# Optimization experiments

Hardware: AMD Instinct MI355X
Metric: run time of the kernel (lower is better)

## Reference

```python
import jax, jax.numpy as jnp
import numpy as np

T, B, I, H = 512, 64, 1024, 1024


def setup_inputs() -> dict:
    key = jax.random.key(0)
    ks = jax.random.split(key, 16)
    d = {
        "inputs": jax.random.normal(ks[0], (T, B, I), dtype=jnp.float32),
        "hx": jnp.zeros((B, H), dtype=jnp.float32),
        "cx": jnp.zeros((B, H), dtype=jnp.float32),
        # weights [H, I] / [H, H] as in nn.Parameter(torch.randn(...)); scaled down for stability
        "w_ii": jax.random.normal(ks[1], (H, I), jnp.float32) * 0.02,
        "w_fi": jax.random.normal(ks[2], (H, I), jnp.float32) * 0.02,
        "w_ai": jax.random.normal(ks[3], (H, I), jnp.float32) * 0.02,
        "w_oi": jax.random.normal(ks[4], (H, I), jnp.float32) * 0.02,
        "w_ih": jax.random.normal(ks[5], (H, H), jnp.float32) * 0.02,
        "w_fh": jax.random.normal(ks[6], (H, H), jnp.float32) * 0.02,
        "w_ah": jax.random.normal(ks[7], (H, H), jnp.float32) * 0.02,
        "w_oh": jax.random.normal(ks[8], (H, H), jnp.float32) * 0.02,
        "b_i": jax.random.uniform(ks[9], (H,), jnp.float32),
        "b_f": jax.random.uniform(ks[10], (H,), jnp.float32),
        "b_a": jax.random.uniform(ks[11], (H,), jnp.float32),
        "b_o": jax.random.normal(ks[12], (H,), jnp.float32),
    }
    return d


def reference(inputs, hx, cx, w_ii, w_fi, w_ai, w_oi, w_ih, w_fh, w_ah, w_oh,
              b_i, b_f, b_a, b_o):
    # FP quant type -> weight proxies and quant activations are identity;
    # layer_norm='identity'; rec_quant/out_quant are IdentityQuant.
    # Stack the 4 gate matrices so each step does one [B,I]x[I,4H] and one
    # [B,H]x[H,4H] GEMM (same math as the 8 separate torch.mm calls).
    Wi = jnp.concatenate([w_ii, w_fi, w_ai, w_oi], axis=0).T  # [I, 4H]
    Wh = jnp.concatenate([w_ih, w_fh, w_ah, w_oh], axis=0).T  # [H, 4H]
    b = jnp.concatenate([b_i, b_f, b_a, b_o], axis=0)          # [4H]
    Hh = hx.shape[-1]

    def step(carry, x_t):
        h, c = carry
        gates = x_t @ Wi + h @ Wh + b                 # [B, 4H]
        i_g, f_g, a_g, o_g = jnp.split(gates, 4, axis=-1)
        i_g = jax.nn.sigmoid(i_g)
        f_g = jax.nn.sigmoid(f_g)
        a_g = jnp.tanh(a_g)
        o_g = jax.nn.sigmoid(o_g)
        cy = f_g * c + i_g * a_g
        hy = o_g * jnp.tanh(cy)
        return (hy, cy), hy

    (hy, cy), outputs = jax.lax.scan(step, (hx, cx), inputs)
    return outputs, hy, cy
```

## Files before the change

kernel.cpp:

```cpp
#include <hip/hip_runtime.h>
#include <cstdint>

typedef _Float16 half8 __attribute__((ext_vector_type(8)));
typedef _Float16 half4v __attribute__((ext_vector_type(4)));
typedef float floatx4 __attribute__((ext_vector_type(4)));
typedef unsigned long long u64;

__device__ __forceinline__ float sig_(float x) { return 1.f / (1.f + __expf(-x)); }
__device__ __forceinline__ float tanh_(float x) {
  x = fminf(15.f, fmaxf(-15.f, x));
  float e = __expf(2.f * x);
  return (e - 1.f) / (e + 1.f);
}

__global__ void cvt_x_kernel(const float* __restrict__ x, _Float16* __restrict__ xh, int n) {
  int i = (blockIdx.x * 256 + threadIdx.x) * 4;
  if (i < n) {
    const float4 v = *(const float4*)(x + i);
    half4v o = {(_Float16)v.x, (_Float16)v.y, (_Float16)v.z, (_Float16)v.w};
    *(half4v*)(xh + i) = o;
  }
}

__global__ void build_w_kernel(const float* w0, const float* w1, const float* w2, const float* w3,
                               const float* w4, const float* w5, const float* w6, const float* w7,
                               const float* b0, const float* b1, const float* b2, const float* b3,
                               _Float16* __restrict__ Wip, _Float16* __restrict__ Whp,
                               float* __restrict__ biasp) {
  int n = blockIdx.x;
  if (n < 8192) {
    const float* srcs[8] = {w0, w1, w2, w3, w4, w5, w6, w7};
    int which = n >> 12;
    int row = n & 4095;
    int u = row >> 2, g = row & 3;
    const float* s = srcs[which * 4 + g] + (size_t)u * 1024;
    _Float16* dst = (which ? Whp : Wip) + (size_t)row * 1024;
    int t = threadIdx.x * 4;
    float4 v = *(const float4*)(s + t);
    half4v o = {(_Float16)v.x, (_Float16)v.y, (_Float16)v.z, (_Float16)v.w};
    *(half4v*)(dst + t) = o;
  } else {
    const float* bs[4] = {b0, b1, b2, b3};
    for (int idx = threadIdx.x; idx < 4096; idx += 256)
      biasp[idx] = bs[idx & 3][idx >> 2];
  }
}

__global__ void init_h_kernel(const float* __restrict__ hx, unsigned int* __restrict__ hbuf) {
  int i = blockIdx.x * 256 + threadIdx.x;
  if (i < 32768) {
    unsigned short lo = __builtin_bit_cast(unsigned short, (_Float16)hx[2 * i]);
    unsigned short hi = __builtin_bit_cast(unsigned short, (_Float16)hx[2 * i + 1]);
    hbuf[i] = (unsigned int)lo | ((unsigned int)hi << 16);
  }
}

__global__ void zero_flags_kernel(unsigned int* __restrict__ flags) {
  int i = blockIdx.x * 256 + threadIdx.x;
  if (i < 8192) flags[i] = 0u;
}

__global__ __launch_bounds__(256) void gemm_g_kernel(const _Float16* __restrict__ Xh,
                                                     const _Float16* __restrict__ Wp,
                                                     const float* __restrict__ biasp,
                                                     _Float16* __restrict__ G3) {
  __shared__ _Float16 Al[4][128][8];
  __shared__ _Float16 Bl[4][128][8];
  const int tid = threadIdx.x;
  const int w = tid >> 6, l = tid & 63;
  const int wm = (w >> 1) * 64, wn = (w & 1) * 64;
  const int ml = l & 15, kg = l >> 4;
  const int bm = blockIdx.x, bn = blockIdx.y;
  const int r0 = tid & 127, kc0 = tid >> 7;
  const int kc1 = kc0 + 2;
  const size_t arow0 = (size_t)(bm * 128 + r0) * 1024;
  const size_t brow0 = (size_t)(bn * 128 + r0) * 1024;
  floatx4 acc[4][4] = {};
  for (int kt = 0; kt < 1024; kt += 32) {
    __syncthreads();
    __builtin_amdgcn_global_load_lds(
        (const __attribute__((address_space(1))) unsigned int*)(Xh + arow0 + kt + kc0 * 8),
        (__attribute__((address_space(3))) unsigned int*)&Al[kc0][r0][0], 16, 0, 0);
    __builtin_amdgcn_global_load_lds(
        (const __attribute__((address_space(1))) unsigned int*)(Xh + arow0 + kt + kc1 * 8),
        (__attribute__((address_space(3))) unsigned int*)&Al[kc1][r0][0], 16, 0, 0);
    __builtin_amdgcn_global_load_lds(
        (const __attribute__((address_space(1))) unsigned int*)(Wp + brow0 + kt + kc0 * 8),
        (__attribute__((address_space(3))) unsigned int*)&Bl[kc0][r0][0], 16, 0, 0);
    __builtin_amdgcn_global_load_lds(
        (const __attribute__((address_space(1))) unsigned int*)(Wp + brow0 + kt + kc1 * 8),
        (__attribute__((address_space(3))) unsigned int*)&Bl[kc1][r0][0], 16, 0, 0);
    __syncthreads();
    half8 af[4], bf[4];
#pragma unroll
    for (int i = 0; i < 4; ++i) af[i] = *(const half8*)&Al[kg][wm + i * 16 + ml][0];
#pragma unroll
    for (int j = 0; j < 4; ++j) bf[j] = *(const half8*)&Bl[kg][wn + j * 16 + ml][0];
#pragma unroll
    for (int i = 0; i < 4; ++i)
#pragma unroll
      for (int j = 0; j < 4; ++j)
        acc[i][j] = __builtin_amdgcn_mfma_f32_16x16x32_f16(af[i], bf[j], acc[i][j], 0, 0, 0);
  }
  const int t = (bm * 128 + wm) >> 6;
#pragma unroll
  for (int j = 0; j < 4; ++j) {
    const int col = bn * 128 + wn + j * 16 + ml;
    const float bj = biasp[col];
    const int p = col >> 4;
#pragma unroll
    for (int i = 0; i < 4; ++i) {
      half4v pk = {(_Float16)(acc[i][j][0] + bj), (_Float16)(acc[i][j][1] + bj),
                   (_Float16)(acc[i][j][2] + bj), (_Float16)(acc[i][j][3] + bj)};
      *(half4v*)&G3[((size_t)p * 512 + t) * 1024 + i * 256 + kg * 64 + ml * 4] = pk;
    }
  }
}

__global__ __launch_bounds__(256, 1) void lstm_rec_kernel(
    const _Float16* __restrict__ G3, const _Float16* __restrict__ Whp,
    unsigned int* __restrict__ hbuf, const float* __restrict__ cx,
    float* __restrict__ out, unsigned int* __restrict__ flags) {
  const int p = blockIdx.x, tid = threadIdx.x;
  const int w = tid >> 6, l = tid & 63;
  const int ml = l & 15, kg = l >> 4;
  __shared__ _Float16 hl_[32768];
  char* hl = (char*)(hl_ + w * 8192);

  half8 wfr[32];
#pragma unroll
  for (int s = 0; s < 32; ++s)
    wfr[s] = *(const half8*)&Whp[(size_t)(16 * p + ml) * 1024 + s * 32 + kg * 8];

  const int bl = l >> 2, u = l & 3;
  const int bglob = 16 * w + bl, U = 4 * p + u;
  float c = cx[bglob * 1024 + U];
  __syncthreads();

  for (int t = 0; t < 512; ++t) {
    const u64* hq = (const u64*)(hbuf + (size_t)(t & 1) * 32768);
    u64* hnq = (u64*)(hbuf + (size_t)((t & 1) ^ 1) * 32768);

    u64 c1[32], c2[32];
#pragma unroll
    for (int i = 0; i < 32; ++i) {
      const int row = i >> 1, j = ((i & 1) << 6) + l;
      c1[i] = __hip_atomic_load(&hq[(size_t)(16 * w + row) * 256 + j], __ATOMIC_RELAXED,
                                __HIP_MEMORY_SCOPE_AGENT);
    }
    const u64 ginb =
        *(const u64*)&G3[((size_t)p * 512 + t) * 1024 + w * 256 + kg * 64 + ml * 4];
#pragma unroll
    for (int i = 0; i < 32; ++i) {
      const int row = i >> 1, j = ((i & 1) << 6) + l;
      c2[i] = __hip_atomic_load(&hq[(size_t)(16 * w + row) * 256 + 128 + j], __ATOMIC_RELAXED,
                                __HIP_MEMORY_SCOPE_AGENT);
    }

#pragma unroll
    for (int i = 0; i < 32; ++i) {
      const int row = i >> 1, j = ((i & 1) << 6) + l;
      const int un = (j >> 1) ^ (row & 7);
      *(u64*)(hl + row * 1024 + un * 16 + (j & 1) * 8) = c1[i];
    }
    __builtin_amdgcn_wave_barrier();
    floatx4 acc[4] = {};
#pragma unroll
    for (int s = 0; s < 16; ++s) {
      const int un = (s * 4 + kg) ^ (ml & 7);
      half8 a = *(const half8*)(hl + ml * 1024 + un * 16);
      acc[s & 3] = __builtin_amdgcn_mfma_f32_16x16x32_f16(a, wfr[s], acc[s & 3], 0, 0, 0);
    }
    __builtin_amdgcn_wave_barrier();
#pragma unroll
    for (int i = 0; i < 32; ++i) {
      const int row = i >> 1, j = ((i & 1) << 6) + l;
      const int un = (j >> 1) ^ (row & 7);
      *(u64*)(hl + row * 1024 + un * 16 + (j & 1) * 8) = c2[i];
    }
    __builtin_amdgcn_wave_barrier();
#pragma unroll
    for (int s = 0; s < 16; ++s) {
      const int un = (s * 4 + kg) ^ (ml & 7);
      half8 a = *(const half8*)(hl + ml * 1024 + un * 16);
      acc[s & 3] = __builtin_amdgcn_mfma_f32_16x16x32_f16(a, wfr[16 + s], acc[s & 3], 0, 0, 0);
    }
    floatx4 a4 = (acc[0] + acc[1]) + (acc[2] + acc[3]);

    union { u64 q; half4v h4; } gu; gu.q = ginb;
    float* glw = (float*)hl;
    __builtin_amdgcn_wave_barrier();
#pragma unroll
    for (int r = 0; r < 4; ++r)
      glw[(kg * 4 + r) * 20 + ml] = a4[r] + (float)gu.h4[r];
    __builtin_amdgcn_wave_barrier();
    const float4 g4 = *(const float4*)&glw[bl * 20 + u * 4];

    const float ig = sig_(g4.x), fg = sig_(g4.y);
    const float ag = tanh_(g4.z), og = sig_(g4.w);
    c = fg * c + ig * ag;
    const float h = og * tanh_(c);

    unsigned int mine = (unsigned int)__builtin_bit_cast(unsigned short, (_Float16)h);
    unsigned int pair = mine | (((unsigned int)__shfl_xor((int)mine, 1)) << 16);
    u64 quad = (u64)pair | ((u64)(unsigned int)__shfl_xor((int)pair, 2) << 32);
    if (u == 0)
      __hip_atomic_store(&hnq[(size_t)bglob * 256 + p], quad, __ATOMIC_RELAXED,
                         __HIP_MEMORY_SCOPE_AGENT);

    if (t == 511) {
      out[(size_t)t * 65536 + bglob * 1024 + U] = h;
      out[(size_t)33554432 + bglob * 1024 + U] = h;
      out[(size_t)33619968 + bglob * 1024 + U] = c;
      break;
    }

    __builtin_amdgcn_s_waitcnt(0x0F70);
    __syncthreads();
    if (tid == 0)
      __hip_atomic_store(&flags[p * 32], (unsigned)(t + 1), __ATOMIC_RELAXED,
                         __HIP_MEMORY_SCOPE_AGENT);
    out[(size_t)t * 65536 + bglob * 1024 + U] = h;
    const unsigned tgt = (unsigned)(t + 1);
    int done;
    do {
      unsigned v = __hip_atomic_load(&flags[tid * 32], __ATOMIC_RELAXED,
                                     __HIP_MEMORY_SCOPE_AGENT);
      done = __syncthreads_and((int)(v >= tgt));
      if (!done) __builtin_amdgcn_s_sleep(2);
    } while (!done);
    asm volatile("" ::: "memory");
  }
}

extern "C" void kernel_launch(void* const* d_in, const int* in_sizes, int n_in,
                              void* d_out, int out_size, void* d_ws, size_t ws_size,
                              hipStream_t stream) {
  const float* x    = (const float*)d_in[0];
  const float* hx   = (const float*)d_in[1];
  const float* cxp  = (const float*)d_in[2];
  const float* w_ii = (const float*)d_in[3];
  const float* w_fi = (const float*)d_in[4];
  const float* w_ai = (const float*)d_in[5];
  const float* w_oi = (const float*)d_in[6];
  const float* w_ih = (const float*)d_in[7];
  const float* w_fh = (const float*)d_in[8];
  const float* w_ah = (const float*)d_in[9];
  const float* w_oh = (const float*)d_in[10];
  const float* b_i  = (const float*)d_in[11];
  const float* b_f  = (const float*)d_in[12];
  const float* b_a  = (const float*)d_in[13];
  const float* b_o  = (const float*)d_in[14];
  float* out = (float*)d_out;

  char* ws = (char*)d_ws;
  _Float16* Xh        = (_Float16*)(ws);
  unsigned int* flags = (unsigned int*)(ws);
  _Float16* Wip       = (_Float16*)(ws + 67108864);
  _Float16* Whp       = (_Float16*)(ws + 75497472);
  float* biasp        = (float*)(ws + 83886080);
  unsigned int* hbuf  = (unsigned int*)(ws + 83902464);
  _Float16* G3        = (_Float16*)(ws + 84164864);
  if (ws_size < (size_t)84164864 + 268435456) return;

  cvt_x_kernel<<<32768, 256, 0, stream>>>(x, Xh, 33554432);
  build_w_kernel<<<8193, 256, 0, stream>>>(w_ii, w_fi, w_ai, w_oi, w_ih, w_fh, w_ah, w_oh,
                                           b_i, b_f, b_a, b_o, Wip, Whp, biasp);
  init_h_kernel<<<128, 256, 0, stream>>>(hx, hbuf);
  gemm_g_kernel<<<dim3(256, 32), 256, 0, stream>>>(Xh, Wip, biasp, G3);
  zero_flags_kernel<<<32, 256, 0, stream>>>(flags);
  lstm_rec_kernel<<<256, 256, 0, stream>>>(G3, Whp, hbuf, cxp, out, flags);
}
```

Measured before the change: 3.805 ms.

## Load hidden state directly into LDS with pre-swizzled layout and faster flag polling

```diff
diff --git a/kernel.cpp b/kernel.cpp
--- a/kernel.cpp
+++ b/kernel.cpp
@@ -46,12 +46,16 @@
   }
 }
 
-__global__ void init_h_kernel(const float* __restrict__ hx, unsigned int* __restrict__ hbuf) {
+__global__ void init_h_kernel(const float* __restrict__ hx, char* __restrict__ hb0) {
   int i = blockIdx.x * 256 + threadIdx.x;
   if (i < 32768) {
-    unsigned short lo = __builtin_bit_cast(unsigned short, (_Float16)hx[2 * i]);
-    unsigned short hi = __builtin_bit_cast(unsigned short, (_Float16)hx[2 * i + 1]);
-    hbuf[i] = (unsigned int)lo | ((unsigned int)hi << 16);
+    int r = i >> 9, j = i & 511;
+    int c = j >> 8, xoff = (j & 255) * 4;
+    int o = (xoff + r * 16) & 1023;
+    unsigned short lo = __builtin_bit_cast(unsigned short, (_Float16)hx[r * 1024 + 2 * j]);
+    unsigned short hi = __builtin_bit_cast(unsigned short, (_Float16)hx[r * 1024 + 2 * j + 1]);
+    *(unsigned int*)(hb0 + (size_t)r * 2048 + c * 1024 + o) =
+        (unsigned int)lo | ((unsigned int)hi << 16);
   }
 }
 
@@ -119,13 +123,13 @@
 
 __global__ __launch_bounds__(256, 1) void lstm_rec_kernel(
     const _Float16* __restrict__ G3, const _Float16* __restrict__ Whp,
-    unsigned int* __restrict__ hbuf, const float* __restrict__ cx,
+    char* __restrict__ hbuf, const float* __restrict__ cx,
     float* __restrict__ out, unsigned int* __restrict__ flags) {
   const int p = blockIdx.x, tid = threadIdx.x;
   const int w = tid >> 6, l = tid & 63;
   const int ml = l & 15, kg = l >> 4;
-  __shared__ _Float16 hl_[32768];
-  char* hl = (char*)(hl_ + w * 8192);
+  __shared__ char hl_[65536] __attribute__((aligned(16)));
+  char* slice = hl_ + w * 16384;
 
   half8 wfr[32];
 #pragma unroll
@@ -135,60 +139,43 @@
   const int bl = l >> 2, u = l & 3;
   const int bglob = 16 * w + bl, U = 4 * p + u;
   float c = cx[bglob * 1024 + U];
+  const int rot = kg * 16 + ml * 16 + w * 256;
   __syncthreads();
 
+  u64 ginb = *(const u64*)&G3[((size_t)p * 512 + 0) * 1024 + w * 256 + kg * 64 + ml * 4];
+
   for (int t = 0; t < 512; ++t) {
-    const u64* hq = (const u64*)(hbuf + (size_t)(t & 1) * 32768);
-    u64* hnq = (u64*)(hbuf + (size_t)((t & 1) ^ 1) * 32768);
-
-    u64 c1[32], c2[32];
-#pragma unroll
-    for (int i = 0; i < 32; ++i) {
-      const int row = i >> 1, j = ((i & 1) << 6) + l;
-      c1[i] = __hip_atomic_load(&hq[(size_t)(16 * w + row) * 256 + j], __ATOMIC_RELAXED,
-                                __HIP_MEMORY_SCOPE_AGENT);
-    }
-    const u64 ginb =
-        *(const u64*)&G3[((size_t)p * 512 + t) * 1024 + w * 256 + kg * 64 + ml * 4];
-#pragma unroll
-    for (int i = 0; i < 32; ++i) {
-      const int row = i >> 1, j = ((i & 1) << 6) + l;
-      c2[i] = __hip_atomic_load(&hq[(size_t)(16 * w + row) * 256 + 128 + j], __ATOMIC_RELAXED,
-                                __HIP_MEMORY_SCOPE_AGENT);
-    }
-
-#pragma unroll
-    for (int i = 0; i < 32; ++i) {
-      const int row = i >> 1, j = ((i & 1) << 6) + l;
-      const int un = (j >> 1) ^ (row & 7);
-      *(u64*)(hl + row * 1024 + un * 16 + (j & 1) * 8) = c1[i];
-    }
-    __builtin_amdgcn_wave_barrier();
+    const char* hq = hbuf + (size_t)(t & 1) * 131072;
+    char* hnq = hbuf + (size_t)((t & 1) ^ 1) * 131072;
+
     floatx4 acc[4] = {};
 #pragma unroll
-    for (int s = 0; s < 16; ++s) {
-      const int un = (s * 4 + kg) ^ (ml & 7);
-      half8 a = *(const half8*)(hl + ml * 1024 + un * 16);
-      acc[s & 3] = __builtin_amdgcn_mfma_f32_16x16x32_f16(a, wfr[s], acc[s & 3], 0, 0, 0);
-    }
-    __builtin_amdgcn_wave_barrier();
-#pragma unroll
-    for (int i = 0; i < 32; ++i) {
-      const int row = i >> 1, j = ((i & 1) << 6) + l;
-      const int un = (j >> 1) ^ (row & 7);
-      *(u64*)(hl + row * 1024 + un * 16 + (j & 1) * 8) = c2[i];
-    }
-    __builtin_amdgcn_wave_barrier();
-#pragma unroll
-    for (int s = 0; s < 16; ++s) {
-      const int un = (s * 4 + kg) ^ (ml & 7);
-      half8 a = *(const half8*)(hl + ml * 1024 + un * 16);
-      acc[s & 3] = __builtin_amdgcn_mfma_f32_16x16x32_f16(a, wfr[16 + s], acc[s & 3], 0, 0, 0);
+    for (int chunk = 0; chunk < 2; ++chunk) {
+#pragma unroll
+      for (int r = 0; r < 16; ++r)
+        __builtin_amdgcn_global_load_lds(
+            (const __attribute__((address_space(1))) unsigned int*)(
+                hq + (size_t)(16 * w + r) * 2048 + chunk * 1024 + l * 16),
+            (__attribute__((address_space(3))) unsigned int*)(slice + r * 1024 + l * 16),
+            16, 0, 0);
+      __builtin_amdgcn_s_waitcnt(0x0F70);
+      __builtin_amdgcn_wave_barrier();
+#pragma unroll
+      for (int s = 0; s < 16; ++s) {
+        const int off = (s * 64 + rot) & 1023;
+        half8 a = *(const half8*)(slice + ml * 1024 + off);
+        acc[s & 3] =
+            __builtin_amdgcn_mfma_f32_16x16x32_f16(a, wfr[chunk * 16 + s], acc[s & 3], 0, 0, 0);
+      }
+      if (chunk == 0) {
+        __builtin_amdgcn_s_waitcnt(0xC07F);
+        __builtin_amdgcn_wave_barrier();
+      }
     }
     floatx4 a4 = (acc[0] + acc[1]) + (acc[2] + acc[3]);
 
     union { u64 q; half4v h4; } gu; gu.q = ginb;
-    float* glw = (float*)hl;
+    float* glw = (float*)slice;
     __builtin_amdgcn_wave_barrier();
 #pragma unroll
     for (int r = 0; r < 4; ++r)
@@ -204,9 +191,12 @@
     unsigned int mine = (unsigned int)__builtin_bit_cast(unsigned short, (_Float16)h);
     unsigned int pair = mine | (((unsigned int)__shfl_xor((int)mine, 1)) << 16);
     u64 quad = (u64)pair | ((u64)(unsigned int)__shfl_xor((int)pair, 2) << 32);
-    if (u == 0)
-      __hip_atomic_store(&hnq[(size_t)bglob * 256 + p], quad, __ATOMIC_RELAXED,
-                         __HIP_MEMORY_SCOPE_AGENT);
+    if (u == 0) {
+      const int hc = p >> 7;
+      const int ho = (((p & 127) * 8) + bglob * 16) & 1023;
+      __hip_atomic_store((u64*)(hnq + (size_t)bglob * 2048 + hc * 1024 + ho), quad,
+                         __ATOMIC_RELAXED, __HIP_MEMORY_SCOPE_AGENT);
+    }
 
     if (t == 511) {
       out[(size_t)t * 65536 + bglob * 1024 + U] = h;
@@ -218,17 +208,26 @@
     __builtin_amdgcn_s_waitcnt(0x0F70);
     __syncthreads();
     if (tid == 0)
-      __hip_atomic_store(&flags[p * 32], (unsigned)(t + 1), __ATOMIC_RELAXED,
+      __hip_atomic_store(&flags[p], (unsigned)(t + 1), __ATOMIC_RELAXED,
                          __HIP_MEMORY_SCOPE_AGENT);
+    u64 gin_next =
+        *(const u64*)&G3[((size_t)p * 512 + (t + 1)) * 1024 + w * 256 + kg * 64 + ml * 4];
     out[(size_t)t * 65536 + bglob * 1024 + U] = h;
-    const unsigned tgt = (unsigned)(t + 1);
-    int done;
-    do {
-      unsigned v = __hip_atomic_load(&flags[tid * 32], __ATOMIC_RELAXED,
-                                     __HIP_MEMORY_SCOPE_AGENT);
-      done = __syncthreads_and((int)(v >= tgt));
-      if (!done) __builtin_amdgcn_s_sleep(2);
-    } while (!done);
+    if (w == 0) {
+      const unsigned tgt = (unsigned)(t + 1);
+      const u64* fq = (const u64*)flags;
+      for (;;) {
+        u64 q0 = __hip_atomic_load(&fq[l], __ATOMIC_RELAXED, __HIP_MEMORY_SCOPE_AGENT);
+        u64 q1 = __hip_atomic_load(&fq[64 + l], __ATOMIC_RELAXED, __HIP_MEMORY_SCOPE_AGENT);
+        int ok = ((unsigned)q0 >= tgt) & ((unsigned)(q0 >> 32) >= tgt) &
+                 ((unsigned)q1 >= tgt) & ((unsigned)(q1 >> 32) >= tgt);
+        if (__all(ok)) break;
+        __builtin_amdgcn_s_sleep(2);
+      }
+    }
+    __syncthreads();
+    __builtin_amdgcn_fence(__ATOMIC_ACQUIRE, "agent");
+    ginb = gin_next;
     asm volatile("" ::: "memory");
   }
 }
@@ -259,7 +258,7 @@
   _Float16* Wip       = (_Float16*)(ws + 67108864);
   _Float16* Whp       = (_Float16*)(ws + 75497472);
   float* biasp        = (float*)(ws + 83886080);
-  unsigned int* hbuf  = (unsigned int*)(ws + 83902464);
+  char* hbuf          = (char*)(ws + 83902464);
   _Float16* G3        = (_Float16*)(ws + 84164864);
   if (ws_size < (size_t)84164864 + 268435456) return;
 
```

After: 8.008 ms. 110% more time.
